# Kernel optimization log

Hardware: AMD Instinct MI355X
Metric: run time of the kernel (lower is better)

## Reference

```python
import jax, jax.numpy as jnp
import numpy as np

D_MODEL = 1024
N_HEADS = 16
HEAD_DIM = D_MODEL // N_HEADS
ROPE_BASE = 10000.0


def rotate_half(x):
    x1, x2 = x[..., : x.shape[-1] // 2], x[..., x.shape[-1] // 2 :]
    return jnp.concatenate((-x2, x1), axis=-1)


def rope_cos_sin(L, dim, dtype):
    inv_freq = 1.0 / (ROPE_BASE ** (jnp.arange(0, dim, 2, dtype=jnp.float32) / dim))
    freqs = jnp.arange(L, dtype=jnp.float32)[:, None] * inv_freq[None, :]  # [L, dim/2]
    emb = jnp.concatenate((freqs, freqs), axis=-1)  # [L, dim]
    # broadcast over batch and heads: [1, L, 1, dim]
    return jnp.cos(emb)[None, :, None, :].astype(dtype), jnp.sin(emb)[None, :, None, :].astype(dtype)


def setup_inputs() -> dict:
    key = jax.random.key(0)
    ks = jax.random.split(key, 11)
    N, L, S = 2, 2048, 2048
    s = 1.0 / np.sqrt(D_MODEL)
    return {
        "queries": jax.random.normal(ks[0], (N, L, D_MODEL), jnp.float32),
        "keys": jax.random.normal(ks[1], (N, S, D_MODEL), jnp.float32),
        "values": jax.random.normal(ks[2], (N, S, D_MODEL), jnp.float32),
        "Wq": jax.random.normal(ks[3], (D_MODEL, D_MODEL), jnp.float32) * s,
        "bq": jnp.zeros((D_MODEL,), jnp.float32),
        "Wk": jax.random.normal(ks[4], (D_MODEL, D_MODEL), jnp.float32) * s,
        "bk": jnp.zeros((D_MODEL,), jnp.float32),
        "Wv": jax.random.normal(ks[5], (D_MODEL, D_MODEL), jnp.float32) * s,
        "bv": jnp.zeros((D_MODEL,), jnp.float32),
        "Wo": jax.random.normal(ks[6], (D_MODEL, D_MODEL), jnp.float32) * s,
        "bo": jnp.zeros((D_MODEL,), jnp.float32),
    }


def reference(queries, keys, values, Wq, bq, Wk, bk, Wv, bv, Wo, bo):
    N, L, _ = queries.shape
    S = keys.shape[1]
    H, hd = N_HEADS, HEAD_DIM

    # QKV projections (nn.Linear: x @ W.T + b), reshape to [N, T, H, hd]
    q = (jnp.einsum("nld,ed->nle", queries, Wq) + bq).reshape(N, L, H, hd)
    k = (jnp.einsum("nsd,ed->nse", keys, Wk) + bk).reshape(N, S, H, hd)
    v = (jnp.einsum("nsd,ed->nse", values, Wv) + bv).reshape(N, S, H, hd)

    # Rotary embedding: q*cos + rotate_half(q)*sin  (same for k)
    cos, sin = rope_cos_sin(L, hd, q.dtype)
    q = q * cos + rotate_half(q) * sin
    k = k * cos + rotate_half(k) * sin

    # Inner attention: scaled dot-product with causal mask
    scores = jnp.einsum("nlhd,nshd->nhls", q, k) / jnp.sqrt(jnp.asarray(hd, q.dtype))
    causal = jnp.tril(jnp.ones((L, S), bool))
    scores = jnp.where(causal[None, None], scores, jnp.asarray(-1e9, scores.dtype))
    attn = jax.nn.softmax(scores, axis=-1)
    out = jnp.einsum("nhls,nshd->nlhd", attn, v).reshape(N, L, H * hd)

    # Output projection
    return jnp.einsum("nle,de->nld", out, Wo) + bo
```

## Files before the change

kernel.cpp:

```cpp
#include <hip/hip_runtime.h>
#include <math.h>

#define DM 1024
#define NH 16
#define HD 64
#define SEQ 2048
#define NB2 2
#define MROWS 4096

typedef unsigned short u16;
typedef __attribute__((ext_vector_type(8))) short short8;
typedef __attribute__((ext_vector_type(4))) float f32x4;
typedef __attribute__((ext_vector_type(2))) unsigned int u32x2;

#define GLOAD16(g, l) __builtin_amdgcn_global_load_lds( \
    (const __attribute__((address_space(1))) void*)(g),  \
    (__attribute__((address_space(3))) void*)(l), 16, 0, 0)

static __device__ __forceinline__ u16 f2bf(float f) {
  union { float f; unsigned u; } v; v.f = f;
  unsigned r = v.u + 0x7fffu + ((v.u >> 16) & 1u);
  return (u16)(r >> 16);
}

static __device__ __forceinline__ short8 cvt8(float4 a, float4 b) {
  short8 s;
  s[0] = (short)f2bf(a.x); s[1] = (short)f2bf(a.y);
  s[2] = (short)f2bf(a.z); s[3] = (short)f2bf(a.w);
  s[4] = (short)f2bf(b.x); s[5] = (short)f2bf(b.y);
  s[6] = (short)f2bf(b.z); s[7] = (short)f2bf(b.w);
  return s;
}

__global__ void conv_all(
    const float* __restrict__ q, const float* __restrict__ k, const float* __restrict__ v,
    const float* __restrict__ wq, const float* __restrict__ wk,
    const float* __restrict__ wv, const float* __restrict__ wo,
    u16* __restrict__ xq, u16* __restrict__ xk, u16* __restrict__ xv,
    u16* __restrict__ wqb, u16* __restrict__ wkb, u16* __restrict__ wvb, u16* __restrict__ wob,
    float* __restrict__ cosT, float* __restrict__ sinT)
{
  const int z = blockIdx.z;
  const int idx = blockIdx.x * blockDim.x + threadIdx.x;
  if (z == 7) {
    if (idx >= SEQ * 32) return;
    int l = idx >> 5, i = idx & 31;
    float invf = expf(-(float)i * (9.210340371976184f / 32.0f));
    float ang = (float)l * invf;
    float s, c;
    sincosf(ang, &s, &c);
    cosT[idx] = c; sinT[idx] = s;
    return;
  }
  const float* src; u16* dst; int n;
  switch (z) {
    case 0: src = q;  dst = xq;  n = MROWS * DM; break;
    case 1: src = k;  dst = xk;  n = MROWS * DM; break;
    case 2: src = v;  dst = xv;  n = MROWS * DM; break;
    case 3: src = wq; dst = wqb; n = DM * DM; break;
    case 4: src = wk; dst = wkb; n = DM * DM; break;
    case 5: src = wv; dst = wvb; n = DM * DM; break;
    default: src = wo; dst = wob; n = DM * DM; break;
  }
  const int base = idx * 8;
  if (base >= n) return;
  float4 a = *(const float4*)(src + base);
  float4 b = *(const float4*)(src + base + 4);
  *(short8*)(dst + base) = cvt8(a, b);
}

__global__ __launch_bounds__(512) void gemm_qkv(
    const u16* __restrict__ Xq, const u16* __restrict__ Xk, const u16* __restrict__ Xv,
    const u16* __restrict__ Wqb, const u16* __restrict__ Wkb, const u16* __restrict__ Wvb,
    const float* __restrict__ bq, const float* __restrict__ bk, const float* __restrict__ bv,
    u16* __restrict__ Qb, u16* __restrict__ Kb, u16* __restrict__ VT,
    const float* __restrict__ cosT, const float* __restrict__ sinT)
{
  __shared__ __align__(16) u16 SH[49152];
  const int z = blockIdx.z;
  const u16* A = (z == 0) ? Xq : (z == 1) ? Xk : Xv;
  const u16* W = (z == 0) ? Wqb : (z == 1) ? Wkb : Wvb;
  const float* bias = (z == 0) ? bq : (z == 1) ? bk : bv;
  const int row0 = blockIdx.x * 256, col0 = blockIdx.y * 256;

  const int tid = threadIdx.x;
  const int lane = tid & 63;
  const int wid = tid >> 6;
  const int wm = wid >> 2;
  const int wn = wid & 3;
  const int fr = lane & 15, kg = lane >> 4;

  const u16* ga = A + (size_t)(row0 + (tid & 255)) * DM + ((tid >> 8) << 3);
  const u16* gb = W + (size_t)(col0 + (tid & 255)) * DM + ((tid >> 8) << 3);
  const int lw = (wid >> 2) * 2048 + (wid & 3) * 512;
  u16* B0 = SH;
  u16* B1 = SH + 16384;
  u16* B2 = SH + 32768;

  f32x4 acc[8][4];
#pragma unroll
  for (int m = 0; m < 8; ++m)
#pragma unroll
    for (int n = 0; n < 4; ++n) acc[m][n] = (f32x4){0.f, 0.f, 0.f, 0.f};

  auto issueA = [&](int t, u16* buf) {
    const int ko = t * 32;
    GLOAD16(ga + ko, buf + lw);
    GLOAD16(ga + ko + 16, buf + lw + 4096);
  };
  auto issueB = [&](int t, u16* buf) {
    const int ko = t * 32;
    GLOAD16(gb + ko, buf + 8192 + lw);
    GLOAD16(gb + ko + 16, buf + 8192 + lw + 4096);
  };

  auto phA = [&](const u16* bufR, u16* bufW, int t2, short8* bfr) {
    short8 afr[4];
#pragma unroll
    for (int m = 0; m < 4; ++m)
      afr[m] = *(const short8*)(&bufR[kg * 2048 + (wm * 128 + m * 16 + fr) * 8]);
#pragma unroll
    for (int n = 0; n < 4; ++n)
      bfr[n] = *(const short8*)(&bufR[8192 + kg * 2048 + (wn * 64 + n * 16 + fr) * 8]);
    if (t2 < 32) issueA(t2, bufW);
    __builtin_amdgcn_sched_barrier(0);
    __builtin_amdgcn_s_barrier();
    __builtin_amdgcn_sched_barrier(0);
    __builtin_amdgcn_s_setprio(1);
#pragma unroll
    for (int m = 0; m < 4; ++m)
#pragma unroll
      for (int n = 0; n < 4; ++n)
        acc[m][n] = __builtin_amdgcn_mfma_f32_16x16x32_bf16(afr[m], bfr[n], acc[m][n], 0, 0, 0);
    __builtin_amdgcn_s_setprio(0);
    __builtin_amdgcn_sched_barrier(0);
    __builtin_amdgcn_s_barrier();
    __builtin_amdgcn_sched_barrier(0);
  };
  auto phB = [&](const u16* bufR, u16* bufW, int t2, const short8* bfr) {
    short8 afr[4];
#pragma unroll
    for (int m = 0; m < 4; ++m)
      afr[m] = *(const short8*)(&bufR[kg * 2048 + (wm * 128 + (m + 4) * 16 + fr) * 8]);
    if (t2 < 32) issueB(t2, bufW);
    __builtin_amdgcn_sched_barrier(0);
    __builtin_amdgcn_s_barrier();
    __builtin_amdgcn_sched_barrier(0);
    __builtin_amdgcn_s_setprio(1);
#pragma unroll
    for (int m = 0; m < 4; ++m)
#pragma unroll
      for (int n = 0; n < 4; ++n)
        acc[m + 4][n] = __builtin_amdgcn_mfma_f32_16x16x32_bf16(afr[m], bfr[n], acc[m + 4][n], 0, 0, 0);
    __builtin_amdgcn_s_setprio(0);
  };

  issueA(0, B0); issueB(0, B0);
  issueA(1, B1); issueB(1, B1);

#define QSTEP(WLIT, bufR, bufW, t2) do {                            \
    asm volatile("s_waitcnt vmcnt(" WLIT ")" ::: "memory");         \
    __builtin_amdgcn_sched_barrier(0);                              \
    __builtin_amdgcn_s_barrier();                                   \
    __builtin_amdgcn_sched_barrier(0);                              \
    short8 bfr[4];                                                  \
    phA(bufR, bufW, t2, bfr);                                       \
    phB(bufR, bufW, t2, bfr);                                       \
  } while (0)

  for (int t = 0; t < 30; t += 3) {
    QSTEP("4", B0, B2, t + 2);
    QSTEP("4", B1, B0, t + 3);
    QSTEP("4", B2, B1, t + 4);
  }
  QSTEP("4", B0, B2, 32);
  QSTEP("0", B1, B2, 33);
#undef QSTEP

  if (z == 2) {
    __syncthreads();
    const int nb = row0 >> 11;
    const int sbase = row0 & (SEQ - 1);
#pragma unroll
    for (int p = 0; p < 4; ++p) {
      if (wn == p) {
#pragma unroll
        for (int n = 0; n < 4; ++n) {
          const int dcol = n * 16 + fr;
          const float bv = bias[col0 + p * 64 + dcol];
#pragma unroll
          for (int m = 0; m < 8; ++m)
#pragma unroll
            for (int r = 0; r < 4; ++r)
              SH[dcol * 264 + wm * 128 + m * 16 + kg * 4 + r] = f2bf(acc[m][n][r] + bv);
        }
      }
      __syncthreads();
      {
        const int dcol = tid >> 3, sq = tid & 7;
        const int e = col0 + p * 64 + dcol;
        u16* dst = VT + ((size_t)(nb * NH + (e >> 6)) * HD + (e & 63)) * SEQ + sbase + sq * 32;
#pragma unroll
        for (int j = 0; j < 4; ++j)
          *(short8*)(dst + j * 8) = *(const short8*)(&SH[dcol * 264 + sq * 32 + j * 8]);
      }
      __syncthreads();
    }
    return;
  }

  const float qscale = (z == 0) ? 0.125f : 1.0f;
  u16* Cb = (z == 0) ? Qb : Kb;
#pragma unroll
  for (int m = 0; m < 8; ++m) {
#pragma unroll
    for (int r = 0; r < 4; ++r) {
      const int rowg = row0 + wm * 128 + m * 16 + kg * 4 + r;
      const int l = rowg & (SEQ - 1);
#pragma unroll
      for (int n = 0; n < 4; ++n) {
        const int colg = col0 + wn * 64 + n * 16 + fr;
        const int i = n * 16 + fr;
        const int fi = i & 31;
        const float c = cosT[l * 32 + fi];
        const float s = sinT[l * 32 + fi];
        const float v = acc[m][n][r] + bias[colg];
        const float pv = acc[m][n ^ 2][r] + bias[col0 + wn * 64 + ((n ^ 2) * 16 + fr)];
        const float o = v * c + ((i < 32) ? -pv : pv) * s;
        Cb[(size_t)rowg * DM + colg] = f2bf(o * qscale);
      }
    }
  }
}

__global__ __launch_bounds__(256) void gemm_o(
    const u16* __restrict__ Ob, const u16* __restrict__ Wob,
    const float* __restrict__ bo, float* __restrict__ out)
{
  __shared__ __align__(16) u16 SH[24576];
  const int row0 = blockIdx.x * 128, col0 = blockIdx.y * 128;
  const int tid = threadIdx.x;
  const int lane = tid & 63;
  const int w = tid >> 6;
  const int wr = w >> 1;
  const int wc = w & 1;
  const int fr = lane & 15, kg = lane >> 4;

  const u16* ga = Ob + (size_t)(row0 + (tid & 127)) * DM + ((tid >> 7) << 3);
  const u16* gb = Wob + (size_t)(col0 + (tid & 127)) * DM + ((tid >> 7) << 3);
  const int lw = w * 512;
  u16* B0 = SH;
  u16* B1 = SH + 8192;
  u16* B2 = SH + 16384;

  f32x4 acc[4][4];
#pragma unroll
  for (int m = 0; m < 4; ++m)
#pragma unroll
    for (int n = 0; n < 4; ++n) acc[m][n] = (f32x4){0.f, 0.f, 0.f, 0.f};

  auto issueA = [&](int t, u16* buf) {
    const int ko = t * 32;
    GLOAD16(ga + ko, buf + lw);
    GLOAD16(ga + ko + 16, buf + lw + 2048);
  };
  auto issueB = [&](int t, u16* buf) {
    const int ko = t * 32;
    GLOAD16(gb + ko, buf + 4096 + lw);
    GLOAD16(gb + ko + 16, buf + 4096 + lw + 2048);
  };

  auto phA = [&](const u16* bufR, u16* bufW, int t2, short8* bfr) {
    short8 afr[2];
#pragma unroll
    for (int m = 0; m < 2; ++m)
      afr[m] = *(const short8*)(&bufR[kg * 1024 + (wr * 64 + m * 16 + fr) * 8]);
#pragma unroll
    for (int n = 0; n < 4; ++n)
      bfr[n] = *(const short8*)(&bufR[4096 + kg * 1024 + (wc * 64 + n * 16 + fr) * 8]);
    if (t2 < 32) issueA(t2, bufW);
    __builtin_amdgcn_sched_barrier(0);
    __builtin_amdgcn_s_barrier();
    __builtin_amdgcn_sched_barrier(0);
    __builtin_amdgcn_s_setprio(1);
#pragma unroll
    for (int m = 0; m < 2; ++m)
#pragma unroll
      for (int n = 0; n < 4; ++n)
        acc[m][n] = __builtin_amdgcn_mfma_f32_16x16x32_bf16(afr[m], bfr[n], acc[m][n], 0, 0, 0);
    __builtin_amdgcn_s_setprio(0);
    __builtin_amdgcn_sched_barrier(0);
    __builtin_amdgcn_s_barrier();
    __builtin_amdgcn_sched_barrier(0);
  };
  auto phB = [&](const u16* bufR, u16* bufW, int t2, const short8* bfr) {
    short8 afr[2];
#pragma unroll
    for (int m = 0; m < 2; ++m)
      afr[m] = *(const short8*)(&bufR[kg * 1024 + (wr * 64 + (m + 2) * 16 + fr) * 8]);
    if (t2 < 32) issueB(t2, bufW);
    __builtin_amdgcn_sched_barrier(0);
    __builtin_amdgcn_s_barrier();
    __builtin_amdgcn_sched_barrier(0);
    __builtin_amdgcn_s_setprio(1);
#pragma unroll
    for (int m = 0; m < 2; ++m)
#pragma unroll
      for (int n = 0; n < 4; ++n)
        acc[m + 2][n] = __builtin_amdgcn_mfma_f32_16x16x32_bf16(afr[m], bfr[n], acc[m + 2][n], 0, 0, 0);
    __builtin_amdgcn_s_setprio(0);
  };

  issueA(0, B0); issueB(0, B0);
  issueA(1, B1); issueB(1, B1);

#define OSTEP(WLIT, bufR, bufW, t2) do {                            \
    asm volatile("s_waitcnt vmcnt(" WLIT ")" ::: "memory");         \
    __builtin_amdgcn_sched_barrier(0);                              \
    __builtin_amdgcn_s_barrier();                                   \
    __builtin_amdgcn_sched_barrier(0);                              \
    short8 bfr[4];                                                  \
    phA(bufR, bufW, t2, bfr);                                       \
    phB(bufR, bufW, t2, bfr);                                       \
  } while (0)

  for (int t = 0; t < 30; t += 3) {
    OSTEP("4", B0, B2, t + 2);
    OSTEP("4", B1, B0, t + 3);
    OSTEP("4", B2, B1, t + 4);
  }
  OSTEP("4", B0, B2, 32);
  OSTEP("0", B1, B2, 33);
#undef OSTEP

#pragma unroll
  for (int m = 0; m < 4; ++m) {
#pragma unroll
    for (int r = 0; r < 4; ++r) {
      const int rowg = row0 + wr * 64 + m * 16 + kg * 4 + r;
#pragma unroll
      for (int n = 0; n < 4; ++n) {
        const int colg = col0 + wc * 64 + n * 16 + fr;
        out[(size_t)rowg * DM + colg] = acc[m][n][r] + bo[colg];
      }
    }
  }
}

__global__ __launch_bounds__(512) void flash_attn(
    const u16* __restrict__ Qp, const u16* __restrict__ Kp,
    const u16* __restrict__ VT, u16* __restrict__ Op)
{
  __shared__ __align__(16) u16 Ks[4096];
  __shared__ __align__(16) u16 Vt[4096];
  __shared__ __align__(16) u16 Pl[9216];

  const int tid = threadIdx.x;
  const int lane = tid & 63;
  const int w = tid >> 6;
  const int fr = lane & 15, rg = lane >> 4;

  const int bid = blockIdx.x;
  const int half = bid >> 8;
  const int p = bid & 255;
  const int qe = half ? (15 - (p & 15)) : (p & 15);
  const int h = p >> 4;
  const int nb = half;

  const size_t headoff = (size_t)nb * SEQ * DM + (size_t)h * HD;
  const size_t vthead = (size_t)(nb * NH + h) * HD * SEQ;
  const int srow = tid >> 3;
  const int sch  = tid & 7;
  u16* Pw = &Pl[w * 1152];

  const int KBend = 2 * qe + 2;
  const int qrow0 = qe * 128 + w * 16;
  const int qg = qrow0 + fr;

  short8 qf[2];
#pragma unroll
  for (int ck = 0; ck < 2; ++ck)
    qf[ck] = *(const short8*)(Qp + headoff + (size_t)(qrow0 + fr) * DM + ck * 32 + rg * 8);

  f32x4 accO[4];
#pragma unroll
  for (int df = 0; df < 4; ++df) accO[df] = (f32x4){0.f, 0.f, 0.f, 0.f};
  float m_run = -3e38f, l_run = 0.f;

  short8 kpf = *(const short8*)(Kp + headoff + (size_t)srow * DM + sch * 8);
  short8 vpf = *(const short8*)(VT + vthead + (size_t)srow * SEQ + sch * 8);

  for (int kb = 0; kb < KBend; ++kb) {
    *(short8*)(&Ks[(sch * 64 + (srow ^ sch)) * 8]) = kpf;
    *(short8*)(&Vt[(sch * 64 + (srow ^ sch)) * 8]) = vpf;
    __syncthreads();
    if (kb + 1 < KBend) {
      kpf = *(const short8*)(Kp + headoff + (size_t)((kb + 1) * 64 + srow) * DM + sch * 8);
      vpf = *(const short8*)(VT + vthead + (size_t)srow * SEQ + (kb + 1) * 64 + sch * 8);
    }

    const bool active = (kb * 64) <= (qrow0 + 15);
    if (active) {
      short8 kf[4][2];
#pragma unroll
      for (int sf = 0; sf < 4; ++sf)
#pragma unroll
        for (int ck = 0; ck < 2; ++ck) {
          const int dc = ck * 4 + rg;
          kf[sf][ck] = *(const short8*)(&Ks[(dc * 64 + ((sf * 16 + fr) ^ dc)) * 8]);
        }
      f32x4 sc_[4];
#pragma unroll
      for (int sf = 0; sf < 4; ++sf) {
        f32x4 z = (f32x4){0.f, 0.f, 0.f, 0.f};
#pragma unroll
        for (int ck = 0; ck < 2; ++ck)
          z = __builtin_amdgcn_mfma_f32_16x16x32_bf16(kf[sf][ck], qf[ck], z, 0, 0, 0);
        sc_[sf] = z;
      }
      float rowmax = -3e38f;
#pragma unroll
      for (int sf = 0; sf < 4; ++sf)
#pragma unroll
        for (int r = 0; r < 4; ++r) {
          const int sg = kb * 64 + sf * 16 + rg * 4 + r;
          float v = sc_[sf][r];
          v = (sg <= qg) ? v : -3e38f;
          sc_[sf][r] = v;
          rowmax = fmaxf(rowmax, v);
        }
      rowmax = fmaxf(rowmax, __shfl_xor(rowmax, 16, 64));
      rowmax = fmaxf(rowmax, __shfl_xor(rowmax, 32, 64));
      const float mnew = fmaxf(m_run, rowmax);
      const float scl = __expf(m_run - mnew);
      m_run = mnew;
      float psum = 0.f;
#pragma unroll
      for (int sf = 0; sf < 4; ++sf)
#pragma unroll
        for (int r = 0; r < 4; ++r) {
          const float pp = __expf(sc_[sf][r] - mnew);
          sc_[sf][r] = pp;
          psum += pp;
        }
      psum += __shfl_xor(psum, 16, 64);
      psum += __shfl_xor(psum, 32, 64);
      l_run = l_run * scl + psum;
      const float s0 = __shfl(scl, rg * 4 + 0, 64);
      const float s1 = __shfl(scl, rg * 4 + 1, 64);
      const float s2 = __shfl(scl, rg * 4 + 2, 64);
      const float s3 = __shfl(scl, rg * 4 + 3, 64);
#pragma unroll
      for (int df = 0; df < 4; ++df) {
        accO[df][0] *= s0; accO[df][1] *= s1;
        accO[df][2] *= s2; accO[df][3] *= s3;
      }
#pragma unroll
      for (int sf = 0; sf < 4; ++sf) {
        u32x2 pv;
        pv[0] = (unsigned)f2bf(sc_[sf][0]) | ((unsigned)f2bf(sc_[sf][1]) << 16);
        pv[1] = (unsigned)f2bf(sc_[sf][2]) | ((unsigned)f2bf(sc_[sf][3]) << 16);
        *(u32x2*)(&Pw[fr * 72 + (sf * 8 + rg * 2) * 2]) = pv;
      }
      short8 pa[2];
#pragma unroll
      for (int ck = 0; ck < 2; ++ck)
        pa[ck] = *(const short8*)(&Pw[fr * 72 + (ck * 16 + rg * 4) * 2]);
#pragma unroll
      for (int df = 0; df < 4; ++df)
#pragma unroll
        for (int ck = 0; ck < 2; ++ck) {
          const int sc = ck * 4 + rg;
          const short8 vf = *(const short8*)(&Vt[(sc * 64 + ((df * 16 + fr) ^ sc)) * 8]);
          accO[df] = __builtin_amdgcn_mfma_f32_16x16x32_bf16(pa[ck], vf, accO[df], 0, 0, 0);
        }
    }
    __syncthreads();
  }

  const float l0 = __shfl(l_run, rg * 4 + 0, 64);
  const float l1 = __shfl(l_run, rg * 4 + 1, 64);
  const float l2 = __shfl(l_run, rg * 4 + 2, 64);
  const float l3 = __shfl(l_run, rg * 4 + 3, 64);
#pragma unroll
  for (int df = 0; df < 4; ++df) {
    const int d = df * 16 + fr;
    Op[headoff + (size_t)(qrow0 + rg * 4 + 0) * DM + d] = f2bf(accO[df][0] / l0);
    Op[headoff + (size_t)(qrow0 + rg * 4 + 1) * DM + d] = f2bf(accO[df][1] / l1);
    Op[headoff + (size_t)(qrow0 + rg * 4 + 2) * DM + d] = f2bf(accO[df][2] / l2);
    Op[headoff + (size_t)(qrow0 + rg * 4 + 3) * DM + d] = f2bf(accO[df][3] / l3);
  }
}

extern "C" void kernel_launch(void* const* d_in, const int* in_sizes, int n_in,
                              void* d_out, int out_size, void* d_ws, size_t ws_size,
                              hipStream_t stream) {
  (void)in_sizes; (void)n_in; (void)out_size; (void)ws_size;
  const float* queries = (const float*)d_in[0];
  const float* keys    = (const float*)d_in[1];
  const float* values  = (const float*)d_in[2];
  const float* Wq = (const float*)d_in[3];
  const float* bq = (const float*)d_in[4];
  const float* Wk = (const float*)d_in[5];
  const float* bk = (const float*)d_in[6];
  const float* Wv = (const float*)d_in[7];
  const float* bv = (const float*)d_in[8];
  const float* Wo = (const float*)d_in[9];
  const float* bo = (const float*)d_in[10];
  float* out = (float*)d_out;

  char* ws = (char*)d_ws;
  const size_t MB = 1u << 20;
  u16* Qb  = (u16*)(ws);
  u16* Kb  = (u16*)(ws + 8 * MB);
  u16* VTg = (u16*)(ws + 16 * MB);
  u16* Xq  = (u16*)(ws + 24 * MB);
  u16* Ob  = Xq;
  u16* Xk  = (u16*)(ws + 32 * MB);
  u16* Xv  = (u16*)(ws + 40 * MB);
  u16* Wqb = (u16*)(ws + 48 * MB);
  u16* Wkb = (u16*)(ws + 50 * MB);
  u16* Wvb = (u16*)(ws + 52 * MB);
  u16* Wob = (u16*)(ws + 54 * MB);
  float* cosT = (float*)(ws + 56 * MB);
  float* sinT = (float*)(ws + 56 * MB + 256 * 1024);

  conv_all<<<dim3(2048, 1, 8), 256, 0, stream>>>(
      queries, keys, values, Wq, Wk, Wv, Wo,
      Xq, Xk, Xv, Wqb, Wkb, Wvb, Wob, cosT, sinT);
  gemm_qkv<<<dim3(MROWS / 256, DM / 256, 3), 512, 0, stream>>>(
      Xq, Xk, Xv, Wqb, Wkb, Wvb, bq, bk, bv, Qb, Kb, VTg, cosT, sinT);
  flash_attn<<<dim3(512, 1, 1), 512, 0, stream>>>(Qb, Kb, VTg, Ob);
  gemm_o<<<dim3(MROWS / 128, DM / 128), 256, 0, stream>>>(Ob, Wob, bo, out);
}
```

Measured before the change: 138.6 us.

## Triple-buffer K/V tiles in flash attention with async global-to-LDS loads

Replaces the register-staged K/V prefetch, which used two block barriers per iteration, with a three-slot LDS ring filled by global_load_lds direct copies issued two tiles ahead. Each iteration waits on the vmcnt counter and uses a single barrier. This is meant to hide global memory latency and remove the register round-trip and one barrier per tile. It raises LDS use to about 66 KB per block, which may lower occupancy. Correctness relies on the lane^w swizzle mapping matching the existing read pattern and on the manual waitcnt being correct.

```diff
diff --git a/kernel.cpp b/kernel.cpp
--- a/kernel.cpp
+++ b/kernel.cpp
@@ -351,8 +351,7 @@
     const u16* __restrict__ Qp, const u16* __restrict__ Kp,
     const u16* __restrict__ VT, u16* __restrict__ Op)
 {
-  __shared__ __align__(16) u16 Ks[4096];
-  __shared__ __align__(16) u16 Vt[4096];
+  __shared__ __align__(16) u16 KV[3][8192];
   __shared__ __align__(16) u16 Pl[9216];
 
   const int tid = threadIdx.x;
@@ -369,14 +368,22 @@
 
   const size_t headoff = (size_t)nb * SEQ * DM + (size_t)h * HD;
   const size_t vthead = (size_t)(nb * NH + h) * HD * SEQ;
-  const int srow = tid >> 3;
-  const int sch  = tid & 7;
   u16* Pw = &Pl[w * 1152];
 
   const int KBend = 2 * qe + 2;
   const int qrow0 = qe * 128 + w * 16;
   const int qg = qrow0 + fr;
 
+  const int srow = lane ^ w;
+  const u16* kga = Kp + headoff + (size_t)srow * DM + w * 8;
+  const u16* vga = VT + vthead + (size_t)srow * SEQ + w * 8;
+  const int ldst = w * 512;
+
+  auto issue = [&](int t, int buf) {
+    GLOAD16(kga + (size_t)(t * 64) * DM, &KV[buf][ldst]);
+    GLOAD16(vga + t * 64, &KV[buf][4096 + ldst]);
+  };
+
   short8 qf[2];
 #pragma unroll
   for (int ck = 0; ck < 2; ++ck)
@@ -387,17 +394,22 @@
   for (int df = 0; df < 4; ++df) accO[df] = (f32x4){0.f, 0.f, 0.f, 0.f};
   float m_run = -3e38f, l_run = 0.f;
 
-  short8 kpf = *(const short8*)(Kp + headoff + (size_t)srow * DM + sch * 8);
-  short8 vpf = *(const short8*)(VT + vthead + (size_t)srow * SEQ + sch * 8);
-
+  issue(0, 0);
+  issue(1, 1);
+
+  int cur = 0;
   for (int kb = 0; kb < KBend; ++kb) {
-    *(short8*)(&Ks[(sch * 64 + (srow ^ sch)) * 8]) = kpf;
-    *(short8*)(&Vt[(sch * 64 + (srow ^ sch)) * 8]) = vpf;
-    __syncthreads();
-    if (kb + 1 < KBend) {
-      kpf = *(const short8*)(Kp + headoff + (size_t)((kb + 1) * 64 + srow) * DM + sch * 8);
-      vpf = *(const short8*)(VT + vthead + (size_t)srow * SEQ + (kb + 1) * 64 + sch * 8);
+    if (kb + 1 < KBend) { asm volatile("s_waitcnt vmcnt(2)" ::: "memory"); }
+    else                { asm volatile("s_waitcnt vmcnt(0)" ::: "memory"); }
+    __builtin_amdgcn_sched_barrier(0);
+    __builtin_amdgcn_s_barrier();
+    __builtin_amdgcn_sched_barrier(0);
+    {
+      int nxt = cur - 1; if (nxt < 0) nxt = 2;
+      if (kb + 2 < KBend) issue(kb + 2, nxt);
     }
+    const u16* Ks = &KV[cur][0];
+    const u16* Vt = &KV[cur][4096];
 
     const bool active = (kb * 64) <= (qrow0 + 15);
     if (active) {
@@ -475,7 +487,7 @@
           accO[df] = __builtin_amdgcn_mfma_f32_16x16x32_bf16(pa[ck], vf, accO[df], 0, 0, 0);
         }
     }
-    __syncthreads();
+    ++cur; if (cur == 3) cur = 0;
   }
 
   const float l0 = __shfl(l_run, rg * 4 + 0, 64);
```

Result: slower. 154.5 us (+11.5%).
